# Optimization experiments

Measured on AMD Instinct MI355X. Metric: run time of the kernel, lower is better.

## Reference

```python
import jax, jax.numpy as jnp
import numpy as np

TEMPERATURE = 0.5
NEG_FILL = -9000000000000000.0


def setup_inputs() -> dict:
    key = jax.random.key(0)
    z = jax.random.normal(key, (16384, 128), dtype=jnp.float32)
    return {"z": z}


def reference(z) -> jnp.ndarray:
    n2 = z.shape[0]  # 2N
    # L2 normalize rows (eps matches torch F.normalize default 1e-12)
    norm = jnp.maximum(jnp.linalg.norm(z, axis=1, keepdims=True), 1e-12)
    zn = z / norm
    # (2N, 2N) cosine similarity scaled by temperature
    sim = jnp.matmul(zn, zn.T) / TEMPERATURE
    # mask self-similarity on the diagonal
    idx = jnp.arange(n2)
    sim = jnp.where(idx[:, None] == idx[None, :], NEG_FILL, sim)
    # positive pair of row i is i^1 (2i <-> 2i+1)
    pos_indices = idx ^ 1
    pos_sim = sim[idx, pos_indices]
    loss = -pos_sim + jax.scipy.special.logsumexp(sim, axis=1)
    return jnp.mean(loss)
```

## Files before the change

kernel.cpp:

```cpp
#include <hip/hip_runtime.h>
#include <hip/hip_bf16.h>

#define N2 16384
#define D  128
#define PANEL 32768
#define SQC1 1.69864360258810896f
#define LN2  0.69314718055994530942f

typedef __bf16 bf16x8 __attribute__((ext_vector_type(8)));
typedef float  f32x4  __attribute__((ext_vector_type(4)));

#if __has_builtin(__builtin_amdgcn_exp2f)
#define EXP2(x) __builtin_amdgcn_exp2f(x)
#else
#define EXP2(x) exp2f(x)
#endif

__device__ __forceinline__ unsigned short f2bf(float f) {
    union { float f; unsigned u; } v; v.f = f;
    unsigned r = v.u + 0x7fffu + ((v.u >> 16) & 1u);
    return (unsigned short)(r >> 16);
}

__device__ __forceinline__ void stage_panel(const char* __restrict__ g,
                                            char* lds, int tid) {
    const int wid = tid >> 6, lane = tid & 63;
    #pragma unroll
    for (int i = 0; i < 8; ++i) {
        int off = (wid << 13) + (i << 10) + (lane << 4);
        int src = off ^ (((off >> 8) & 7) << 4);
        __builtin_amdgcn_global_load_lds(
            (const __attribute__((address_space(1))) unsigned*)(g + src),
            (__attribute__((address_space(3))) unsigned*)(lds + (wid << 13) + (i << 10)),
            16, 0, 0);
    }
}

__global__ void k_norm(const float* __restrict__ z, unsigned short* __restrict__ zn,
                       float* __restrict__ rowsum, float* __restrict__ posparts,
                       float* __restrict__ out) {
    __shared__ float xs[4][64][2];
    __shared__ float ps[4];
    if (blockIdx.x < 64) rowsum[blockIdx.x * 256 + threadIdx.x] = 0.f;
    if (blockIdx.x == 64 && threadIdx.x == 0) out[0] = 0.f;
    int wid  = threadIdx.x >> 6, lane = threadIdx.x & 63;
    int row  = blockIdx.x * 4 + wid;
    const float2 v = ((const float2*)(z + (size_t)row * D))[lane];
    float ss = v.x * v.x + v.y * v.y;
    #pragma unroll
    for (int m = 1; m < 64; m <<= 1) ss += __shfl_xor(ss, m);
    float inv = SQC1 / fmaxf(sqrtf(ss), 1e-12f);
    float nx = v.x * inv, ny = v.y * inv;
    ushort2 o; o.x = f2bf(nx); o.y = f2bf(ny);
    ((ushort2*)(zn + (size_t)row * D))[lane] = o;

    xs[wid][lane][0] = nx; xs[wid][lane][1] = ny;
    __syncthreads();
    float d = nx * xs[wid ^ 1][lane][0] + ny * xs[wid ^ 1][lane][1];
    #pragma unroll
    for (int m = 1; m < 64; m <<= 1) d += __shfl_xor(d, m);
    if (lane == 0) ps[wid] = d;
    __syncthreads();
    if (threadIdx.x == 0)
        posparts[blockIdx.x] = ps[0] + ps[1] + ps[2] + ps[3];
}

__global__ __launch_bounds__(256, 2)
void k_sim(const unsigned short* __restrict__ zn, float* __restrict__ rowsum) {
    __shared__ unsigned short ls[2][PANEL / 2];
    char* ls0 = (char*)&ls[0][0];
    char* ls1 = (char*)&ls[1][0];

    const int tileI = blockIdx.y;
    const int sBase = blockIdx.x * 16;
    const int nt = (blockIdx.x == 3 && tileI < 64) ? 17 : 16;
    const int tid  = threadIdx.x;
    const int lane = tid & 63, wid = tid >> 6;
    const int wr = wid >> 1, wc = wid & 1;
    const int l16 = lane & 15, lg = lane >> 4;
    const char* znb = (const char*)zn;
    const f32x4 ZERO = {0.f, 0.f, 0.f, 0.f};

    stage_panel(znb + (size_t)tileI * PANEL, ls0, tid);
    stage_panel(znb + (size_t)((tileI + sBase) & 127) * PANEL, ls1, tid);
    asm volatile("s_waitcnt vmcnt(8)" ::: "memory");
    __builtin_amdgcn_s_barrier();

    bf16x8 af[4][4];
    #pragma unroll
    for (int kk = 0; kk < 4; ++kk)
        #pragma unroll
        for (int m = 0; m < 4; ++m) {
            int row = wr * 64 + m * 16 + l16;
            int d = row * 256 + kk * 64 + lg * 16;
            af[kk][m] = *(const bf16x8*)(ls0 + (d ^ ((row & 7) << 4)));
        }
    asm volatile("s_waitcnt lgkmcnt(0)" ::: "memory");
    __builtin_amdgcn_s_barrier();

    float rs[4][4];
    #pragma unroll
    for (int m = 0; m < 4; ++m)
        #pragma unroll
        for (int r = 0; r < 4; ++r) rs[m][r] = 0.f;

    for (int t = 0; t < nt; ++t) {
        const int s  = sBase + t;
        const int jt = (tileI + s) & 127;
        char* rbuf = (t & 1) ? ls0 : ls1;
        char* sbuf = (t & 1) ? ls1 : ls0;
        if (t < nt - 1) {
            stage_panel(znb + (size_t)((tileI + s + 1) & 127) * PANEL, sbuf, tid);
            asm volatile("s_waitcnt vmcnt(8)" ::: "memory");
        } else {
            asm volatile("s_waitcnt vmcnt(0)" ::: "memory");
        }
        __builtin_amdgcn_s_barrier();

        bf16x8 bfr[4][4];
        #pragma unroll
        for (int kk = 0; kk < 4; ++kk)
            #pragma unroll
            for (int n = 0; n < 4; ++n) {
                int row = wc * 64 + n * 16 + l16;
                int d = row * 256 + kk * 64 + lg * 16;
                bfr[kk][n] = *(const bf16x8*)(rbuf + (d ^ ((row & 7) << 4)));
            }
        asm volatile("s_waitcnt lgkmcnt(0)" ::: "memory");
        __builtin_amdgcn_s_barrier();

        f32x4 acc[4][4];
        #pragma unroll
        for (int m = 0; m < 4; ++m)
            #pragma unroll
            for (int n = 0; n < 4; ++n)
                acc[m][n] = __builtin_amdgcn_mfma_f32_16x16x32_bf16(af[0][m], bfr[0][n], ZERO, 0, 0, 0);
        #pragma unroll
        for (int kk = 1; kk < 4; ++kk)
            #pragma unroll
            for (int m = 0; m < 4; ++m)
                #pragma unroll
                for (int n = 0; n < 4; ++n)
                    acc[m][n] = __builtin_amdgcn_mfma_f32_16x16x32_bf16(af[kk][m], bfr[kk][n], acc[m][n], 0, 0, 0);

        if (s == 0) {
            #pragma unroll
            for (int m = 0; m < 4; ++m)
                #pragma unroll
                for (int r = 0; r < 4; ++r) {
                    int li = wr * 64 + m * 16 + lg * 4 + r;
                    float a = 0.f;
                    #pragma unroll
                    for (int n = 0; n < 4; ++n) {
                        int lj = wc * 64 + n * 16 + l16;
                        float e = EXP2(acc[m][n][r]);
                        a += (li == lj) ? 0.f : e;
                    }
                    rs[m][r] += a;
                }
        } else {
            float cs[4] = {0.f, 0.f, 0.f, 0.f};
            #pragma unroll
            for (int m = 0; m < 4; ++m)
                #pragma unroll
                for (int r = 0; r < 4; ++r) {
                    float a = 0.f;
                    #pragma unroll
                    for (int n = 0; n < 4; ++n) {
                        float e = EXP2(acc[m][n][r]);
                        a += e;
                        cs[n] += e;
                    }
                    rs[m][r] += a;
                }
            #pragma unroll
            for (int n = 0; n < 4; ++n) {
                float v = cs[n];
                v += __shfl_xor(v, 16);
                v += __shfl_xor(v, 32);
                if (lg == 0)
                    atomicAdd(&rowsum[jt * 128 + wc * 64 + n * 16 + l16], v);
            }
        }
    }

    #pragma unroll
    for (int m = 0; m < 4; ++m)
        #pragma unroll
        for (int r = 0; r < 4; ++r) {
            float v = rs[m][r];
            v += __shfl_xor(v, 1);
            v += __shfl_xor(v, 2);
            v += __shfl_xor(v, 4);
            v += __shfl_xor(v, 8);
            if (l16 == 0)
                atomicAdd(&rowsum[tileI * 128 + wr * 64 + m * 16 + lg * 4 + r], v);
        }
}

__global__ void k_loss_reduce(const float* __restrict__ rowsum,
                              const float* __restrict__ posparts,
                              float* __restrict__ out) {
    const int tid = threadIdx.x + blockIdx.x * 256;
    float part = logf(rowsum[tid]);
    if (blockIdx.x == 0) {
        float pp = 0.f;
        for (int i = threadIdx.x; i < N2 / 4; i += 256) pp += posparts[i];
        part -= LN2 * pp;
    }
    __shared__ float sm[4];
    #pragma unroll
    for (int m = 1; m < 64; m <<= 1) part += __shfl_xor(part, m);
    if ((threadIdx.x & 63) == 0) sm[threadIdx.x >> 6] = part;
    __syncthreads();
    if (threadIdx.x == 0)
        atomicAdd(out, (sm[0] + sm[1] + sm[2] + sm[3]) * (1.0f / (float)N2));
}

extern "C" void kernel_launch(void* const* d_in, const int* in_sizes, int n_in,
                              void* d_out, int out_size, void* d_ws, size_t ws_size,
                              hipStream_t stream) {
    const float* z = (const float*)d_in[0];
    float* out = (float*)d_out;

    unsigned short* zn = (unsigned short*)d_ws;
    float* rowsum   = (float*)((char*)d_ws + (size_t)N2 * D * 2);
    float* posparts = rowsum + N2;

    k_norm<<<N2 / 4, 256, 0, stream>>>(z, zn, rowsum, posparts, out);
    dim3 grid(4, 128);
    k_sim<<<grid, 256, 0, stream>>>(zn, rowsum);
    k_loss_reduce<<<64, 256, 0, stream>>>(rowsum, posparts, out);
}
```

Baseline: 62.45 us.

## Use 256-row A tiles with 512-thread blocks sharing each staged B panel

```diff
diff --git a/kernel.cpp b/kernel.cpp
--- a/kernel.cpp
+++ b/kernel.cpp
@@ -3,7 +3,8 @@
 
 #define N2 16384
 #define D  128
-#define PANEL 32768
+#define APANEL 65536
+#define BPANEL 32768
 #define SQC1 1.69864360258810896f
 #define LN2  0.69314718055994530942f
 
@@ -22,17 +23,30 @@
     return (unsigned short)(r >> 16);
 }
 
-__device__ __forceinline__ void stage_panel(const char* __restrict__ g,
-                                            char* lds, int tid) {
+__device__ __forceinline__ void stage_A(const char* __restrict__ g,
+                                        char* ls0, char* ls1, int tid) {
     const int wid = tid >> 6, lane = tid & 63;
     #pragma unroll
     for (int i = 0; i < 8; ++i) {
-        int off = (wid << 13) + (i << 10) + (lane << 4);
-        int src = off ^ (((off >> 8) & 7) << 4);
+        int o = (wid << 13) + (i << 10) + (lane << 4);
+        int src = o ^ (((o >> 8) & 7) << 4);
+        char* dst = (wid < 4) ? (ls0 + o) : (ls1 + (o - 32768));
         __builtin_amdgcn_global_load_lds(
             (const __attribute__((address_space(1))) unsigned*)(g + src),
-            (__attribute__((address_space(3))) unsigned*)(lds + (wid << 13) + (i << 10)),
-            16, 0, 0);
+            (__attribute__((address_space(3))) unsigned*)dst, 16, 0, 0);
+    }
+}
+
+__device__ __forceinline__ void stage_B(const char* __restrict__ g,
+                                        char* lds, int tid) {
+    const int wid = tid >> 6, lane = tid & 63;
+    #pragma unroll
+    for (int i = 0; i < 4; ++i) {
+        int o = (wid << 12) + (i << 10) + (lane << 4);
+        int src = o ^ (((o >> 8) & 7) << 4);
+        __builtin_amdgcn_global_load_lds(
+            (const __attribute__((address_space(1))) unsigned*)(g + src),
+            (__attribute__((address_space(3))) unsigned*)(lds + o), 16, 0, 0);
     }
 }
 
@@ -65,15 +79,16 @@
         posparts[blockIdx.x] = ps[0] + ps[1] + ps[2] + ps[3];
 }
 
-__global__ __launch_bounds__(256, 2)
+__global__ __launch_bounds__(512, 4)
 void k_sim(const unsigned short* __restrict__ zn, float* __restrict__ rowsum) {
-    __shared__ unsigned short ls[2][PANEL / 2];
+    __shared__ unsigned short ls[2][BPANEL / 2];
     char* ls0 = (char*)&ls[0][0];
     char* ls1 = (char*)&ls[1][0];
 
-    const int tileI = blockIdx.y;
-    const int sBase = blockIdx.x * 16;
-    const int nt = (blockIdx.x == 3 && tileI < 64) ? 17 : 16;
+    const int ti = blockIdx.y;
+    const int c  = blockIdx.x;
+    const int nt = (c == 0) ? 10 : 8;
+
     const int tid  = threadIdx.x;
     const int lane = tid & 63, wid = tid >> 6;
     const int wr = wid >> 1, wc = wid & 1;
@@ -81,23 +96,30 @@
     const char* znb = (const char*)zn;
     const f32x4 ZERO = {0.f, 0.f, 0.f, 0.f};
 
-    stage_panel(znb + (size_t)tileI * PANEL, ls0, tid);
-    stage_panel(znb + (size_t)((tileI + sBase) & 127) * PANEL, ls1, tid);
-    asm volatile("s_waitcnt vmcnt(8)" ::: "memory");
+    stage_A(znb + (size_t)ti * APANEL, ls0, ls1, tid);
+    asm volatile("s_waitcnt vmcnt(0)" ::: "memory");
     __builtin_amdgcn_s_barrier();
 
     bf16x8 af[4][4];
-    #pragma unroll
-    for (int kk = 0; kk < 4; ++kk)
-        #pragma unroll
-        for (int m = 0; m < 4; ++m) {
-            int row = wr * 64 + m * 16 + l16;
-            int d = row * 256 + kk * 64 + lg * 16;
-            af[kk][m] = *(const bf16x8*)(ls0 + (d ^ ((row & 7) << 4)));
-        }
+    {
+        char* abase = (wr < 2) ? ls0 : ls1;
+        #pragma unroll
+        for (int kk = 0; kk < 4; ++kk)
+            #pragma unroll
+            for (int m = 0; m < 4; ++m) {
+                int rowl = ((wr & 1) * 64) + m * 16 + l16;
+                int d = rowl * 256 + kk * 64 + lg * 16;
+                af[kk][m] = *(const bf16x8*)(abase + (d ^ ((rowl & 7) << 4)));
+            }
+    }
     asm volatile("s_waitcnt lgkmcnt(0)" ::: "memory");
     __builtin_amdgcn_s_barrier();
 
+    {
+        int s0v = (c == 0) ? 0 : c * 8;
+        stage_B(znb + (size_t)((2 * ti + s0v) & 127) * BPANEL, ls0, tid);
+    }
+
     float rs[4][4];
     #pragma unroll
     for (int m = 0; m < 4; ++m)
@@ -105,13 +127,14 @@
         for (int r = 0; r < 4; ++r) rs[m][r] = 0.f;
 
     for (int t = 0; t < nt; ++t) {
-        const int s  = sBase + t;
-        const int jt = (tileI + s) & 127;
-        char* rbuf = (t & 1) ? ls0 : ls1;
-        char* sbuf = (t & 1) ? ls1 : ls0;
+        const int s  = (c == 0 && t >= 8) ? (56 + t) : (c * 8 + t);
+        const int jt = (2 * ti + s) & 127;
+        char* rbuf = (t & 1) ? ls1 : ls0;
+        char* sbuf = (t & 1) ? ls0 : ls1;
         if (t < nt - 1) {
-            stage_panel(znb + (size_t)((tileI + s + 1) & 127) * PANEL, sbuf, tid);
-            asm volatile("s_waitcnt vmcnt(8)" ::: "memory");
+            const int s1v = (c == 0 && t + 1 >= 8) ? (56 + t + 1) : (c * 8 + t + 1);
+            stage_B(znb + (size_t)((2 * ti + s1v) & 127) * BPANEL, sbuf, tid);
+            asm volatile("s_waitcnt vmcnt(4)" ::: "memory");
         } else {
             asm volatile("s_waitcnt vmcnt(0)" ::: "memory");
         }
@@ -143,43 +166,52 @@
                 for (int n = 0; n < 4; ++n)
                     acc[m][n] = __builtin_amdgcn_mfma_f32_16x16x32_bf16(af[kk][m], bfr[kk][n], acc[m][n], 0, 0, 0);
 
-        if (s == 0) {
-            #pragma unroll
-            for (int m = 0; m < 4; ++m)
-                #pragma unroll
-                for (int r = 0; r < 4; ++r) {
-                    int li = wr * 64 + m * 16 + lg * 4 + r;
-                    float a = 0.f;
+        const bool low = (wr < 2);
+        const bool s1f = (s == 1), s64f = (s == 64), s65f = (s == 65);
+        bool active = low ? (!(s1f || s65f) && !(s64f && ti >= 32))
+                          : (!(s65f && ti >= 32));
+        const bool diag = (s == 0 && low) || (s1f && !low);
+        const int dBase = s1f ? 128 : 0;
+
+        if (active) {
+            if (diag) {
+                #pragma unroll
+                for (int m = 0; m < 4; ++m)
                     #pragma unroll
-                    for (int n = 0; n < 4; ++n) {
-                        int lj = wc * 64 + n * 16 + l16;
-                        float e = EXP2(acc[m][n][r]);
-                        a += (li == lj) ? 0.f : e;
+                    for (int r = 0; r < 4; ++r) {
+                        int li = wr * 64 + m * 16 + lg * 4 + r;
+                        float a = 0.f;
+                        #pragma unroll
+                        for (int n = 0; n < 4; ++n) {
+                            int lj = wc * 64 + n * 16 + l16;
+                            float e = EXP2(acc[m][n][r]);
+                            a += (li == dBase + lj) ? 0.f : e;
+                        }
+                        rs[m][r] += a;
                     }
-                    rs[m][r] += a;
+            } else {
+                float cs[4] = {0.f, 0.f, 0.f, 0.f};
+                #pragma unroll
+                for (int m = 0; m < 4; ++m)
+                    #pragma unroll
+                    for (int r = 0; r < 4; ++r) {
+                        float a = 0.f;
+                        #pragma unroll
+                        for (int n = 0; n < 4; ++n) {
+                            float e = EXP2(acc[m][n][r]);
+                            a += e;
+                            cs[n] += e;
+                        }
+                        rs[m][r] += a;
+                    }
+                #pragma unroll
+                for (int n = 0; n < 4; ++n) {
+                    float v = cs[n];
+                    v += __shfl_xor(v, 16);
+                    v += __shfl_xor(v, 32);
+                    if (lg == 0)
+                        atomicAdd(&rowsum[jt * 128 + wc * 64 + n * 16 + l16], v);
                 }
-        } else {
-            float cs[4] = {0.f, 0.f, 0.f, 0.f};
-            #pragma unroll
-            for (int m = 0; m < 4; ++m)
-                #pragma unroll
-                for (int r = 0; r < 4; ++r) {
-                    float a = 0.f;
-                    #pragma unroll
-                    for (int n = 0; n < 4; ++n) {
-                        float e = EXP2(acc[m][n][r]);
-                        a += e;
-                        cs[n] += e;
-                    }
-                    rs[m][r] += a;
-                }
-            #pragma unroll
-            for (int n = 0; n < 4; ++n) {
-                float v = cs[n];
-                v += __shfl_xor(v, 16);
-                v += __shfl_xor(v, 32);
-                if (lg == 0)
-                    atomicAdd(&rowsum[jt * 128 + wc * 64 + n * 16 + l16], v);
             }
         }
     }
@@ -194,7 +226,7 @@
             v += __shfl_xor(v, 4);
             v += __shfl_xor(v, 8);
             if (l16 == 0)
-                atomicAdd(&rowsum[tileI * 128 + wr * 64 + m * 16 + lg * 4 + r], v);
+                atomicAdd(&rowsum[ti * 256 + wr * 64 + m * 16 + lg * 4 + r], v);
         }
 }
 
@@ -228,7 +260,7 @@
     float* posparts = rowsum + N2;
 
     k_norm<<<N2 / 4, 256, 0, stream>>>(z, zn, rowsum, posparts, out);
-    dim3 grid(4, 128);
-    k_sim<<<grid, 256, 0, stream>>>(zn, rowsum);
+    dim3 grid(8, 64);
+    k_sim<<<grid, 512, 0, stream>>>(zn, rowsum);
     k_loss_reduce<<<64, 256, 0, stream>>>(rowsum, posparts, out);
 }
```

Result: slower. 203.5 us (+225.8%).
